# Kernel optimization log

Hardware: AMD Instinct MI355X
Metric: run time of the kernel (lower is better)

## Reference

```python
import jax, jax.numpy as jnp
import numpy as np

B, D, U = 8192, 1024, 1024

def setup_inputs() -> dict:
    key = jax.random.key(0)
    ks = jax.random.split(key, 20)
    s = 0.02
    inp = {
        'x': jax.random.normal(ks[0], (B, D), jnp.float32),
        'h': jax.random.normal(ks[1], (B, U), jnp.float32),
        'c': jax.random.normal(ks[2], (B, U), jnp.float32),
        'W_i': jax.random.normal(ks[3], (D, U), jnp.float32) * s,
        'W_f': jax.random.normal(ks[4], (D, U), jnp.float32) * s,
        'W_c': jax.random.normal(ks[5], (D, U), jnp.float32) * s,
        'W_o': jax.random.normal(ks[6], (D, U), jnp.float32) * s,
        'U_i': jax.random.normal(ks[7], (U, U), jnp.float32) * s,
        'U_f': jax.random.normal(ks[8], (U, U), jnp.float32) * s,
        'U_c': jax.random.normal(ks[9], (U, U), jnp.float32) * s,
        'U_o': jax.random.normal(ks[10], (U, U), jnp.float32) * s,
        'V_i': jnp.ones((U,), jnp.float32),
        'V_f': jnp.ones((U,), jnp.float32),
        'V_o': jnp.ones((U,), jnp.float32),
        'b_i': jnp.zeros((U,), jnp.float32),
        'b_f': jnp.ones((U,), jnp.float32),
        'b_c': jnp.zeros((U,), jnp.float32),
        'b_o': jnp.zeros((U,), jnp.float32),
    }
    return inp


def reference(x, h, c, W_i, W_f, W_c, W_o, U_i, U_f, U_c, U_o,
              V_i, V_f, V_o, b_i, b_f, b_c, b_o):
    # Fuse the 4 input and 4 recurrent projections into two GEMMs.
    W = jnp.concatenate([W_i, W_f, W_c, W_o], axis=1)   # [D, 4U]
    Uw = jnp.concatenate([U_i, U_f, U_c, U_o], axis=1)  # [U, 4U]
    b = jnp.concatenate([b_i, b_f, b_c, b_o])           # [4U]
    z = x @ W + h @ Uw + b                               # [B, 4U]
    zi, zf, zc, zo = jnp.split(z, 4, axis=1)
    i_t = jax.nn.sigmoid(zi + V_i * c)
    f_t = jax.nn.sigmoid(zf + V_f * c)
    c_tilde = jnp.tanh(zc)
    c_t = f_t * c + i_t * c_tilde
    o_t = jax.nn.sigmoid(zo + V_o * c_t)
    h_t = o_t * jnp.tanh(c_t)
    return (h_t, c_t)
```

## Files before the change

kernel.cpp:

```cpp
#include <hip/hip_runtime.h>
#include <hip/hip_bf16.h>
#include <stdint.h>


#define MM 8192
#define KK 2048
#define NN 4096
#define BM 128
#define BN 128
#define BK 64

typedef __attribute__((ext_vector_type(8))) __bf16 bf16x8;
typedef __attribute__((ext_vector_type(4))) float floatx4;
typedef __attribute__((ext_vector_type(8))) unsigned short ushort8_t;

__device__ __forceinline__ unsigned short f2bf(float f) {
    unsigned int u = __float_as_uint(f);
    u += 0x7FFF + ((u >> 16) & 1);
    return (unsigned short)(u >> 16);
}

__device__ __forceinline__ float fast_sigmoid(float x) {
    return 1.0f / (1.0f + __expf(-x));
}

__device__ __forceinline__ float fast_tanh(float x) {
    float ax = fabsf(x);
    float e = __expf(-2.0f * ax);
    float t = (1.0f - e) / (1.0f + e);
    return copysignf(t, x);
}

__device__ __forceinline__ void async_copy16(const void* g, void* l) {
    __builtin_amdgcn_global_load_lds(
        (const __attribute__((address_space(1))) void*)g,
        (__attribute__((address_space(3))) void*)l,
        16, 0, 0);
}

__global__ void pack_A(const float* __restrict__ x, const float* __restrict__ h,
                       unsigned short* __restrict__ A) {
    int t = blockIdx.x * 256 + threadIdx.x;
    long base = (long)t * 8;
    int row = (int)(base >> 11);
    int col = (int)(base & 2047);
    const float* src = (col < 1024) ? (x + (long)row * 1024 + col)
                                    : (h + (long)row * 1024 + (col - 1024));
    float4 v0 = *(const float4*)src;
    float4 v1 = *(const float4*)(src + 4);
    ushort8_t o;
    o[0] = f2bf(v0.x); o[1] = f2bf(v0.y); o[2] = f2bf(v0.z); o[3] = f2bf(v0.w);
    o[4] = f2bf(v1.x); o[5] = f2bf(v1.y); o[6] = f2bf(v1.z); o[7] = f2bf(v1.w);
    *(ushort8_t*)(A + base) = o;
}

__global__ void pack_W(const float* __restrict__ Wi, const float* __restrict__ Wf,
                       const float* __restrict__ Wc, const float* __restrict__ Wo,
                       const float* __restrict__ Ui, const float* __restrict__ Uf,
                       const float* __restrict__ Uc, const float* __restrict__ Uo,
                       unsigned short* __restrict__ Wt) {
    __shared__ float tile[64][65];
    int z = blockIdx.z;
    const float* src;
    switch (z) {
        case 0: src = Wi; break; case 1: src = Wf; break;
        case 2: src = Wc; break; case 3: src = Wo; break;
        case 4: src = Ui; break; case 5: src = Uf; break;
        case 6: src = Uc; break; default: src = Uo; break;
    }
    int g = z & 3;
    int koff = (z >= 4) ? 1024 : 0;
    int d0 = blockIdx.x * 64;
    int u0 = blockIdx.y * 64;
    int tid = threadIdx.x;

    int j = tid & 63;
    int ib = tid >> 6;
#pragma unroll
    for (int p = 0; p < 16; ++p) {
        int i = p * 4 + ib;
        tile[i][j] = src[(long)(d0 + i) * 1024 + u0 + j];
    }
    __syncthreads();
    int i2 = (tid & 31) * 2;
    int jb = tid >> 5;
#pragma unroll
    for (int p = 0; p < 8; ++p) {
        int j2 = p * 8 + jb;
        unsigned short a = f2bf(tile[i2][j2]);
        unsigned short b = f2bf(tile[i2 + 1][j2]);
        long orow = (long)((u0 + j2) * 4 + g);
        *(ushort2*)(Wt + orow * 2048 + koff + d0 + i2) = make_ushort2(a, b);
    }
}

__global__ __launch_bounds__(256) void lstm_gemm(
    const unsigned short* __restrict__ A,
    const unsigned short* __restrict__ Wt,
    const float* __restrict__ c_in,
    const float* __restrict__ Vi, const float* __restrict__ Vf, const float* __restrict__ Vo,
    const float* __restrict__ bi_p, const float* __restrict__ bf_p,
    const float* __restrict__ bc_p, const float* __restrict__ bo_p,
    float* __restrict__ out) {
    __shared__ __align__(16) char smem[32768];
    unsigned short* As = (unsigned short*)smem;
    unsigned short* Bs = (unsigned short*)(smem + 16384);

    int tid = threadIdx.x;
    int wave = tid >> 6;
    int lane = tid & 63;
    int wm = wave >> 1, wn = wave & 1;

    int id = blockIdx.x;
    int by = (id >> 3) & 31;
    int bx = (id & 7) | ((id >> 8) << 3);
    int rm0 = bx * BM;
    int cn0 = by * BN;

    int r_l = lane >> 3;
    int kc = ((lane & 7) ^ r_l) * 8;
    const unsigned short* gA = A + (long)(rm0 + wave * 32 + r_l) * 2048 + kc;
    const unsigned short* gB = Wt + (long)(cn0 + wave * 32 + r_l) * 2048 + kc;
    char* ldsA = smem + wave * 4096;
    char* ldsB = smem + 16384 + wave * 4096;

    int fr = lane & 15;
    int fc = lane >> 4;
    int m7 = fr & 7;

    floatx4 acc[4][4];
#pragma unroll
    for (int i = 0; i < 4; ++i)
#pragma unroll
        for (int j = 0; j < 4; ++j) acc[i][j] = (floatx4)(0.0f);

    for (int kt = 0; kt < KK / BK; ++kt) {
        int k0 = kt * BK;
#pragma unroll
        for (int c8 = 0; c8 < 4; ++c8)
            async_copy16(gA + (long)(c8 * 8) * 2048 + k0, ldsA + c8 * 1024);
#pragma unroll
        for (int c8 = 0; c8 < 4; ++c8)
            async_copy16(gB + (long)(c8 * 8) * 2048 + k0, ldsB + c8 * 1024);
        __syncthreads();

#pragma unroll
        for (int ks = 0; ks < 2; ++ks) {
            int sl = ((ks * 4 + fc) ^ m7) * 8;
            bf16x8 af[4], bfr[4];
#pragma unroll
            for (int mi = 0; mi < 4; ++mi)
                af[mi] = *(const bf16x8*)(As + (wm * 64 + mi * 16 + fr) * 64 + sl);
#pragma unroll
            for (int ni = 0; ni < 4; ++ni)
                bfr[ni] = *(const bf16x8*)(Bs + (wn * 64 + ni * 16 + fr) * 64 + sl);
#pragma unroll
            for (int mi = 0; mi < 4; ++mi)
#pragma unroll
                for (int ni = 0; ni < 4; ++ni)
                    acc[mi][ni] = __builtin_amdgcn_mfma_f32_16x16x32_bf16(
                        af[mi], bfr[ni], acc[mi][ni], 0, 0, 0);
        }
        __syncthreads();
    }

    float* zs = (float*)(smem) + wave * 1088;
    int u_loc = lane & 15;
    int u_glob = by * 32 + wn * 16 + u_loc;
    int q = lane >> 4;
    float vVi = Vi[u_glob], vVf = Vf[u_glob], vVo = Vo[u_glob];
    float vbi = bi_p[u_glob], vbf = bf_p[u_glob], vbc = bc_p[u_glob], vbo = bo_p[u_glob];

#pragma unroll
    for (int mi = 0; mi < 4; ++mi) {
        __syncthreads();
#pragma unroll
        for (int ni = 0; ni < 4; ++ni)
#pragma unroll
            for (int r = 0; r < 4; ++r)
                zs[(q * 4 + r) * 68 + ni * 16 + u_loc] = acc[mi][ni][r];
        __syncthreads();
#pragma unroll
        for (int t = 0; t < 4; ++t) {
            int rr = t * 4 + q;
            floatx4 z4 = *(const floatx4*)(zs + rr * 68 + u_loc * 4);
            long row_glob = rm0 + wm * 64 + mi * 16 + rr;
            float cv = c_in[row_glob * 1024 + u_glob];
            float i_t = fast_sigmoid(z4[0] + vbi + vVi * cv);
            float f_t = fast_sigmoid(z4[1] + vbf + vVf * cv);
            float ctl = fast_tanh(z4[2] + vbc);
            float c_t = f_t * cv + i_t * ctl;
            float o_t = fast_sigmoid(z4[3] + vbo + vVo * c_t);
            float h_t = o_t * fast_tanh(c_t);
            out[row_glob * 1024 + u_glob] = h_t;
            out[8388608 + row_glob * 1024 + u_glob] = c_t;
        }
    }
}

extern "C" void kernel_launch(void* const* d_in, const int* in_sizes, int n_in,
                              void* d_out, int out_size, void* d_ws, size_t ws_size,
                              hipStream_t stream) {
    const float* x  = (const float*)d_in[0];
    const float* h  = (const float*)d_in[1];
    const float* c  = (const float*)d_in[2];
    const float* Wi = (const float*)d_in[3];
    const float* Wf = (const float*)d_in[4];
    const float* Wc = (const float*)d_in[5];
    const float* Wo = (const float*)d_in[6];
    const float* Ui = (const float*)d_in[7];
    const float* Uf = (const float*)d_in[8];
    const float* Uc = (const float*)d_in[9];
    const float* Uo = (const float*)d_in[10];
    const float* Vi = (const float*)d_in[11];
    const float* Vf = (const float*)d_in[12];
    const float* Vo = (const float*)d_in[13];
    const float* bi = (const float*)d_in[14];
    const float* bf = (const float*)d_in[15];
    const float* bc = (const float*)d_in[16];
    const float* bo = (const float*)d_in[17];

    unsigned short* Abf = (unsigned short*)d_ws;
    unsigned short* Wt  = (unsigned short*)((char*)d_ws + 33554432);

    pack_A<<<dim3(8192), 256, 0, stream>>>(x, h, Abf);
    pack_W<<<dim3(16, 16, 8), 256, 0, stream>>>(Wi, Wf, Wc, Wo, Ui, Uf, Uc, Uo, Wt);
    lstm_gemm<<<dim3(2048), 256, 0, stream>>>(Abf, Wt, c, Vi, Vf, Vo,
                                              bi, bf, bc, bo, (float*)d_out);
}
```

Baseline: 352.3 us.

## Merge pack kernels, change tile ordering, and widen epilogue row coalescing

Combines the activation and weight packing kernels into a single launch to cut one kernel launch and its tail. The GEMM block mapping becomes a simple column-major order (64 row tiles per column tile), replacing the grouped swizzle, which changes L2 reuse of the weight tiles. The global address arithmetic is split into a uniform base plus a per-lane offset to reduce 64-bit address math. The epilogue stages the whole 32x128 tile in shared memory so each thread handles 32 consecutive units, which gives wider contiguous c loads and output stores.

```diff
diff --git a/kernel.cpp b/kernel.cpp
--- a/kernel.cpp
+++ b/kernel.cpp
@@ -38,29 +38,33 @@
         16, 0, 0);
 }
 
-__global__ void pack_A(const float* __restrict__ x, const float* __restrict__ h,
-                       unsigned short* __restrict__ A) {
-    int t = blockIdx.x * 256 + threadIdx.x;
-    long base = (long)t * 8;
-    int row = (int)(base >> 11);
-    int col = (int)(base & 2047);
-    const float* src = (col < 1024) ? (x + (long)row * 1024 + col)
-                                    : (h + (long)row * 1024 + (col - 1024));
-    float4 v0 = *(const float4*)src;
-    float4 v1 = *(const float4*)(src + 4);
-    ushort8_t o;
-    o[0] = f2bf(v0.x); o[1] = f2bf(v0.y); o[2] = f2bf(v0.z); o[3] = f2bf(v0.w);
-    o[4] = f2bf(v1.x); o[5] = f2bf(v1.y); o[6] = f2bf(v1.z); o[7] = f2bf(v1.w);
-    *(ushort8_t*)(A + base) = o;
-}
-
-__global__ void pack_W(const float* __restrict__ Wi, const float* __restrict__ Wf,
-                       const float* __restrict__ Wc, const float* __restrict__ Wo,
-                       const float* __restrict__ Ui, const float* __restrict__ Uf,
-                       const float* __restrict__ Uc, const float* __restrict__ Uo,
-                       unsigned short* __restrict__ Wt) {
+__global__ void pack_all(const float* __restrict__ x, const float* __restrict__ h,
+                         const float* __restrict__ Wi, const float* __restrict__ Wf,
+                         const float* __restrict__ Wc, const float* __restrict__ Wo,
+                         const float* __restrict__ Ui, const float* __restrict__ Uf,
+                         const float* __restrict__ Uc, const float* __restrict__ Uo,
+                         unsigned short* __restrict__ A,
+                         unsigned short* __restrict__ Wt) {
     __shared__ float tile[64][65];
-    int z = blockIdx.z;
+    int blk = blockIdx.x;
+    int tid = threadIdx.x;
+    if (blk >= 2048) {
+        int t = (blk - 2048) * 256 + tid;
+        long base = (long)t * 8;
+        int row = (int)(base >> 11);
+        int col = (int)(base & 2047);
+        const float* src = (col < 1024) ? (x + (long)row * 1024 + col)
+                                        : (h + (long)row * 1024 + (col - 1024));
+        float4 v0 = *(const float4*)src;
+        float4 v1 = *(const float4*)(src + 4);
+        ushort8_t o;
+        o[0] = f2bf(v0.x); o[1] = f2bf(v0.y); o[2] = f2bf(v0.z); o[3] = f2bf(v0.w);
+        o[4] = f2bf(v1.x); o[5] = f2bf(v1.y); o[6] = f2bf(v1.z); o[7] = f2bf(v1.w);
+        *(ushort8_t*)(A + base) = o;
+        return;
+    }
+    int z = blk >> 8;
+    int rem = blk & 255;
     const float* src;
     switch (z) {
         case 0: src = Wi; break; case 1: src = Wf; break;
@@ -70,9 +74,8 @@
     }
     int g = z & 3;
     int koff = (z >= 4) ? 1024 : 0;
-    int d0 = blockIdx.x * 64;
-    int u0 = blockIdx.y * 64;
-    int tid = threadIdx.x;
+    int d0 = (rem >> 4) * 64;
+    int u0 = (rem & 15) * 64;
 
     int j = tid & 63;
     int ib = tid >> 6;
@@ -112,15 +115,16 @@
     int wm = wave >> 1, wn = wave & 1;
 
     int id = blockIdx.x;
-    int by = (id >> 3) & 31;
-    int bx = (id & 7) | ((id >> 8) << 3);
+    int bx = id & 63;
+    int by = id >> 6;
     int rm0 = bx * BM;
     int cn0 = by * BN;
 
     int r_l = lane >> 3;
     int kc = ((lane & 7) ^ r_l) * 8;
-    const unsigned short* gA = A + (long)(rm0 + wave * 32 + r_l) * 2048 + kc;
-    const unsigned short* gB = Wt + (long)(cn0 + wave * 32 + r_l) * 2048 + kc;
+    const unsigned short* gAu = A + (long)rm0 * 2048;
+    const unsigned short* gBu = Wt + (long)cn0 * 2048;
+    int voff = (wave * 32 + r_l) * 2048 + kc;
     char* ldsA = smem + wave * 4096;
     char* ldsB = smem + 16384 + wave * 4096;
 
@@ -136,12 +140,14 @@
 
     for (int kt = 0; kt < KK / BK; ++kt) {
         int k0 = kt * BK;
+        const unsigned short* gAk = gAu + k0;
+        const unsigned short* gBk = gBu + k0;
 #pragma unroll
         for (int c8 = 0; c8 < 4; ++c8)
-            async_copy16(gA + (long)(c8 * 8) * 2048 + k0, ldsA + c8 * 1024);
+            async_copy16(gAk + voff + c8 * (8 * 2048), ldsA + c8 * 1024);
 #pragma unroll
         for (int c8 = 0; c8 < 4; ++c8)
-            async_copy16(gB + (long)(c8 * 8) * 2048 + k0, ldsB + c8 * 1024);
+            async_copy16(gBk + voff + c8 * (8 * 2048), ldsB + c8 * 1024);
         __syncthreads();
 
 #pragma unroll
@@ -164,27 +170,28 @@
         __syncthreads();
     }
 
-    float* zs = (float*)(smem) + wave * 1088;
-    int u_loc = lane & 15;
-    int u_glob = by * 32 + wn * 16 + u_loc;
+    float* zs = (float*)smem;
+    int col = lane & 15;
     int q = lane >> 4;
+    int u_b = tid & 31;
+    int u_glob = by * 32 + u_b;
     float vVi = Vi[u_glob], vVf = Vf[u_glob], vVo = Vo[u_glob];
     float vbi = bi_p[u_glob], vbf = bf_p[u_glob], vbc = bc_p[u_glob], vbo = bo_p[u_glob];
 
 #pragma unroll
     for (int mi = 0; mi < 4; ++mi) {
+        if (mi) __syncthreads();
+#pragma unroll
+        for (int ni = 0; ni < 4; ++ni)
+#pragma unroll
+            for (int r = 0; r < 4; ++r)
+                zs[(wm * 16 + q * 4 + r) * 132 + wn * 64 + ni * 16 + col] = acc[mi][ni][r];
         __syncthreads();
 #pragma unroll
-        for (int ni = 0; ni < 4; ++ni)
-#pragma unroll
-            for (int r = 0; r < 4; ++r)
-                zs[(q * 4 + r) * 68 + ni * 16 + u_loc] = acc[mi][ni][r];
-        __syncthreads();
-#pragma unroll
         for (int t = 0; t < 4; ++t) {
-            int rr = t * 4 + q;
-            floatx4 z4 = *(const floatx4*)(zs + rr * 68 + u_loc * 4);
-            long row_glob = rm0 + wm * 64 + mi * 16 + rr;
+            int rowL = (tid >> 5) + t * 8;
+            floatx4 z4 = *(const floatx4*)(zs + rowL * 132 + u_b * 4);
+            long row_glob = rm0 + (rowL >> 4) * 64 + mi * 16 + (rowL & 15);
             float cv = c_in[row_glob * 1024 + u_glob];
             float i_t = fast_sigmoid(z4[0] + vbi + vVi * cv);
             float f_t = fast_sigmoid(z4[1] + vbf + vVf * cv);
@@ -223,8 +230,8 @@
     unsigned short* Abf = (unsigned short*)d_ws;
     unsigned short* Wt  = (unsigned short*)((char*)d_ws + 33554432);
 
-    pack_A<<<dim3(8192), 256, 0, stream>>>(x, h, Abf);
-    pack_W<<<dim3(16, 16, 8), 256, 0, stream>>>(Wi, Wf, Wc, Wo, Ui, Uf, Uc, Uo, Wt);
+    pack_all<<<dim3(10240), 256, 0, stream>>>(x, h, Wi, Wf, Wc, Wo,
+                                              Ui, Uf, Uc, Uo, Abf, Wt);
     lstm_gemm<<<dim3(2048), 256, 0, stream>>>(Abf, Wt, c, Vi, Vf, Vo,
                                               bi, bf, bc, bo, (float*)d_out);
 }
```

Result: faster. 343.5 us (-2.5%).
